# Optimization experiments

Hardware: AMD Instinct MI355X
Metric: run time of the kernel (lower is better)

## Reference

```python
import jax, jax.numpy as jnp
import numpy as np

DECAY = 0.8
BETA = 0.25
EPS = 1e-05
CODEBOOK_SIZE = 16384
CODEBOOK_DIM = 256


def setup_inputs() -> dict:
    key = jax.random.key(0)
    k1, k2 = jax.random.split(key)
    z = jax.random.normal(k1, (16, 256, 32, 32), dtype=jnp.float32)
    # EmbeddingEMA init: weight = randn(K, D) / K; embed_avg = weight.clone(); cluster_size = 0
    weight = jax.random.normal(k2, (CODEBOOK_SIZE, CODEBOOK_DIM), dtype=jnp.float32) / CODEBOOK_SIZE
    cluster_size = jnp.zeros((CODEBOOK_SIZE,), dtype=jnp.float32)
    embed_avg = weight
    return {"z": z, "weight": weight, "cluster_size": cluster_size, "embed_avg": embed_avg}


def reference(z, weight, cluster_size, embed_avg):
    K, D = weight.shape
    # b c h w -> b h w c
    zt = jnp.transpose(z, (0, 2, 3, 1))
    zf = zt.reshape(-1, D)  # [N, D]

    # squared-distance matrix [N, K]: |z|^2 + |w|^2 - 2 z.wT
    d = (jnp.sum(zf * zf, axis=1, keepdims=True)
         + jnp.sum(weight * weight, axis=1)
         - 2.0 * jnp.einsum('nd,kd->nk', zf, weight))
    token = jnp.argmin(d, axis=1)  # [N]

    z_q = weight[token].reshape(zt.shape)  # embedding lookup

    # training-mode EMA updates (scatter-add of one-hot assignments)
    counts = jax.ops.segment_sum(jnp.ones_like(token, dtype=zf.dtype), token, num_segments=K)
    embed_sum = jax.ops.segment_sum(zf, token, num_segments=K)  # one_hot.T @ zf
    cluster_new = DECAY * cluster_size + (1.0 - DECAY) * counts
    embed_avg_new = DECAY * embed_avg + (1.0 - DECAY) * embed_sum
    n = jnp.sum(cluster_new)
    smoothed = (cluster_new + EPS) / (n + K * EPS) * n
    weight_new = embed_avg_new / smoothed[:, None]

    # commitment loss (z_q detached)
    loss = BETA * jnp.mean((jax.lax.stop_gradient(z_q) - zt) ** 2)
    # straight-through estimator
    z_q_ste = zt + jax.lax.stop_gradient(z_q - zt)
    quant_error = jnp.mean(jnp.sum((z_q - zt) ** 2, axis=3))

    # codebook stats
    utilization = jnp.sum((counts > 0).astype(jnp.float32)) / K
    avg_probs = counts / jnp.sum(counts)
    perplexity = jnp.exp(-jnp.sum(avg_probs * jnp.log(avg_probs + 1e-10)))

    out = jnp.transpose(z_q_ste, (0, 3, 1, 2))  # b h w c -> b c h w
    return (out, loss, quant_error, utilization, perplexity,
            weight_new, cluster_new, embed_avg_new)
```

## Files before the change

### kernel.cpp

```cpp
#include <hip/hip_runtime.h>

#define N_TOK 16384
#define KCB   16384
#define DIM   256
#define HW    1024
#define DECAYF 0.8f
#define ONE_M_DECAY 0.2f
#define BETAF 0.25f
#define EPSF  1e-5f
#define STRIPS 8
#define KB_PER 16

typedef __attribute__((ext_vector_type(8))) short bf16x8;
typedef __attribute__((ext_vector_type(4))) float f32x4;

__device__ __forceinline__ float wave_reduce_sum(float s) {
    #pragma unroll
    for (int o = 32; o > 0; o >>= 1) s += __shfl_down(s, o);
    return s;
}

__device__ __forceinline__ unsigned short f2bf(float x) {
    union { float f; unsigned int u; } a; a.f = x;
    unsigned int r = a.u + 0x7fffu + ((a.u >> 16) & 1u);
    return (unsigned short)(r >> 16);
}

__global__ void k_transpose_z(const float* __restrict__ z, float* __restrict__ zf,
                              unsigned short* __restrict__ Ah) {
    __shared__ float t[32][33];
    int b  = blockIdx.z;
    int c0 = blockIdx.y * 32;
    int h0 = blockIdx.x * 32;
    int tid = threadIdx.x;
    int jx = tid & 31, iy = tid >> 5;
    const float* zb = z + (size_t)b * DIM * HW;
    #pragma unroll
    for (int p = 0; p < 4; ++p) {
        int ci = iy + p * 8;
        t[ci][jx] = zb[(size_t)(c0 + ci) * HW + h0 + jx];
    }
    __syncthreads();
    #pragma unroll
    for (int p = 0; p < 4; ++p) {
        int hh = iy + p * 8;
        size_t idx = (size_t)(b * HW + h0 + hh) * DIM + c0 + jx;
        float v = t[jx][hh];
        zf[idx] = v;
        Ah[idx] = f2bf(v);
    }
}

__global__ void k_prep_w(const float* __restrict__ w, unsigned short* __restrict__ Bh,
                         float* __restrict__ wnorm) {
    int wv = blockIdx.x * 4 + (threadIdx.x >> 6);
    int lane = threadIdx.x & 63;
    float4 v = ((const float4*)(w + (size_t)wv * DIM))[lane];
    ushort4 h;
    h.x = f2bf(v.x); h.y = f2bf(v.y); h.z = f2bf(v.z); h.w = f2bf(v.w);
    ((ushort4*)(Bh + (size_t)wv * DIM))[lane] = h;
    float s = v.x * v.x + v.y * v.y + v.z * v.z + v.w * v.w;
    s = wave_reduce_sum(s);
    if (lane == 0) wnorm[wv] = s;
}

__global__ void k_sum_cs(const float* __restrict__ cs, float* __restrict__ scal) {
    int i = blockIdx.x * 256 + threadIdx.x;
    int lane = threadIdx.x & 63;
    float v = cs[i];
    v = wave_reduce_sum(v);
    if (lane == 0) atomicAdd(&scal[1], v);
}

__global__ __launch_bounds__(256) void k_gemm_argmin(
    const unsigned short* __restrict__ Ah, const unsigned short* __restrict__ Bh,
    const float* __restrict__ wnorm, uint2* __restrict__ pout) {
    __shared__ unsigned short As[128 * 256];
    __shared__ unsigned short Bs[128 * 32];

    int tid  = threadIdx.x;
    int wave = tid >> 6, lane = tid & 63;
    int g16  = lane >> 4, r16 = lane & 15;
    int n0   = blockIdx.x * 128;
    int strip = blockIdx.y;

    #pragma unroll
    for (int i = 0; i < 16; ++i) {
        int s = (wave * 16 + i) * 64 + lane;
        int row = s >> 5, pos = s & 31;
        int c = pos ^ (row & 7);
        const unsigned int* ga = (const unsigned int*)(Ah + (size_t)(n0 + row) * 256 + c * 8);
        unsigned int* la = (unsigned int*)&As[(size_t)((wave * 16 + i) * 64) * 8];
        __builtin_amdgcn_global_load_lds((const __attribute__((address_space(1))) unsigned int*)ga,
                                         (__attribute__((address_space(3))) unsigned int*)la, 16, 0, 0);
    }

    unsigned int b1[16], b2[16];
    #pragma unroll
    for (int i = 0; i < 16; ++i) { b1[i] = 0xFFFFFFFFu; b2[i] = 0xFFFFFFFFu; }

    for (int kbi = 0; kbi < KB_PER; ++kbi) {
        int kb = strip * KB_PER + kbi;
        int c0 = kb * 128;

        f32x4 acc[4][4];
        #pragma unroll
        for (int mt = 0; mt < 4; ++mt)
            #pragma unroll
            for (int nt = 0; nt < 4; ++nt)
                acc[mt][nt] = (f32x4){0.f, 0.f, 0.f, 0.f};

        for (int ks = 0; ks < 8; ++ks) {
            __syncthreads();
            #pragma unroll
            for (int j = 0; j < 2; ++j) {
                int s = (wave * 2 + j) * 64 + lane;
                int m = s >> 2, pk = (s & 3) ^ (m & 3);
                const unsigned int* gb = (const unsigned int*)(Bh + (size_t)(c0 + m) * 256 + ks * 32 + pk * 8);
                unsigned int* lb = (unsigned int*)&Bs[(size_t)((wave * 2 + j) * 64) * 8];
                __builtin_amdgcn_global_load_lds((const __attribute__((address_space(1))) unsigned int*)gb,
                                                 (__attribute__((address_space(3))) unsigned int*)lb, 16, 0, 0);
            }
            __syncthreads();
            bf16x8 af[4], bfr[4];
            #pragma unroll
            for (int mt = 0; mt < 4; ++mt) {
                int row = (wave >> 1) * 64 + mt * 16 + r16;
                int pos = (ks * 4 + g16) ^ (row & 7);
                af[mt] = *(const bf16x8*)&As[(row * 32 + pos) * 8];
            }
            #pragma unroll
            for (int nt = 0; nt < 4; ++nt) {
                int row = (wave & 1) * 64 + nt * 16 + r16;
                int pk = g16 ^ (row & 3);
                bfr[nt] = *(const bf16x8*)&Bs[(row * 4 + pk) * 8];
            }
            #pragma unroll
            for (int mt = 0; mt < 4; ++mt)
                #pragma unroll
                for (int nt = 0; nt < 4; ++nt)
                    acc[mt][nt] = __builtin_amdgcn_mfma_f32_16x16x32_bf16(af[mt], bfr[nt], acc[mt][nt], 0, 0, 0);
        }

        float wnb[4];
        unsigned int orv[4];
        #pragma unroll
        for (int nt = 0; nt < 4; ++nt) {
            int code = c0 + (wave & 1) * 64 + nt * 16 + r16;
            wnb[nt] = wnorm[code] + 0.0625f;
            orv[nt] = (unsigned int)((kbi << 7) | ((wave & 1) << 6) | (nt << 4));
        }
        #pragma unroll
        for (int mt = 0; mt < 4; ++mt)
            #pragma unroll
            for (int rg = 0; rg < 4; ++rg) {
                int i = mt * 4 + rg;
                #pragma unroll
                for (int nt = 0; nt < 4; ++nt) {
                    float s = fmaf(-2.0f, acc[mt][nt][rg], wnb[nt]);
                    unsigned int u = (__float_as_uint(s) & 0xFFFFF800u) | orv[nt];
                    unsigned int t = b1[i] > u ? b1[i] : u;
                    b1[i] = b1[i] < u ? b1[i] : u;
                    b2[i] = b2[i] < t ? b2[i] : t;
                }
            }
    }

    #pragma unroll
    for (int i = 0; i < 16; ++i) {
        unsigned int v1 = b1[i] | (unsigned int)r16;
        unsigned int v2 = b2[i] | (unsigned int)r16;
        #pragma unroll
        for (int off = 1; off < 16; off <<= 1) {
            unsigned int o1 = __shfl_xor((int)v1, off);
            unsigned int o2 = __shfl_xor((int)v2, off);
            unsigned int n1 = v1 < o1 ? v1 : o1;
            unsigned int hi = v1 < o1 ? o1 : v1;
            unsigned int lo = v2 < o2 ? v2 : o2;
            v1 = n1;
            v2 = hi < lo ? hi : lo;
        }
        b1[i] = v1; b2[i] = v2;
    }

    __syncthreads();
    unsigned int* red1 = (unsigned int*)Bs;
    unsigned int* red2 = red1 + 256;
    if (r16 == 0) {
        #pragma unroll
        for (int mt = 0; mt < 4; ++mt)
            #pragma unroll
            for (int rg = 0; rg < 4; ++rg) {
                int row = (wave >> 1) * 64 + mt * 16 + g16 * 4 + rg;
                red1[(wave & 1) * 128 + row] = b1[mt * 4 + rg];
                red2[(wave & 1) * 128 + row] = b2[mt * 4 + rg];
            }
    }
    __syncthreads();
    if (tid < 128) {
        unsigned int a1 = red1[tid], a2 = red2[tid];
        unsigned int c1 = red1[128 + tid], c2 = red2[128 + tid];
        unsigned int m1 = a1 < c1 ? a1 : c1;
        unsigned int hi = a1 < c1 ? c1 : a1;
        unsigned int lo = a2 < c2 ? a2 : c2;
        pout[(size_t)strip * N_TOK + n0 + tid] = make_uint2(m1, hi < lo ? hi : lo);
    }
}

__global__ void k_select(const uint2* __restrict__ pout, const float* __restrict__ zf,
                         const float* __restrict__ w, int2* __restrict__ tokrank,
                         float* __restrict__ counts, float* __restrict__ dmin) {
    int n = blockIdx.x * 4 + (threadIdx.x >> 6);
    int lane = threadIdx.x & 63;
    unsigned int c1 = 0xFFFFFFFFu, c2 = 0xFFFFFFFFu;
    int s1 = 0, s2 = 0;
    #pragma unroll
    for (int s = 0; s < STRIPS; ++s) {
        uint2 p = pout[(size_t)s * N_TOK + n];
        if (p.x < c1)      { c2 = c1; s2 = s1; c1 = p.x; s1 = s; }
        else if (p.x < c2) { c2 = p.x; s2 = s; }
        if (p.y < c1)      { c2 = c1; s2 = s1; c1 = p.y; s1 = s; }
        else if (p.y < c2) { c2 = p.y; s2 = s; }
    }
    int code1 = (s1 << 11) | (int)(c1 & 0x7FFu);
    int code2 = (s2 << 11) | (int)(c2 & 0x7FFu);

    float4 zv = ((const float4*)(zf + (size_t)n * DIM))[lane];
    float4 w1 = ((const float4*)(w + (size_t)code1 * DIM))[lane];
    float4 w2 = ((const float4*)(w + (size_t)code2 * DIM))[lane];
    float ax = zv.x - w1.x, ay = zv.y - w1.y, az = zv.z - w1.z, aw = zv.w - w1.w;
    float bx = zv.x - w2.x, by = zv.y - w2.y, bz = zv.z - w2.z, bw = zv.w - w2.w;
    float d1 = ax * ax + ay * ay + az * az + aw * aw;
    float d2 = bx * bx + by * by + bz * bz + bw * bw;
    d1 = wave_reduce_sum(d1);
    d2 = wave_reduce_sum(d2);
    if (lane == 0) {
        bool take2 = (d2 < d1) || (d2 == d1 && code2 < code1);
        int tok = take2 ? code2 : code1;
        dmin[n] = take2 ? d2 : d1;
        float old = atomicAdd(&counts[tok], 1.0f);
        tokrank[n] = make_int2(tok, (int)old);
    }
}

__global__ void k_scan(const float* __restrict__ counts, int* __restrict__ offsets) {
    int tid = threadIdx.x;
    int lane = tid & 63, wv = tid >> 6;
    int base = tid * 64;
    int sum = 0;
    for (int i = 0; i < 64; ++i) sum += (int)counts[base + i];
    int x = sum;
    #pragma unroll
    for (int o = 1; o < 64; o <<= 1) {
        int y = __shfl_up(x, o);
        if (lane >= o) x += y;
    }
    __shared__ int wt[4];
    if (lane == 63) wt[wv] = x;
    __syncthreads();
    int wbase = 0;
    for (int i = 0; i < wv; ++i) wbase += wt[i];
    int run = wbase + x - sum;
    for (int i = 0; i < 64; ++i) {
        offsets[base + i] = run;
        run += (int)counts[base + i];
    }
}

__global__ void k_scatter(const int2* __restrict__ tokrank, const int* __restrict__ offsets,
                          int* __restrict__ perm) {
    int n = blockIdx.x * 256 + threadIdx.x;
    int2 tr = tokrank[n];
    perm[offsets[tr.x] + tr.y] = n;
}

__global__ void k_embed(const int* __restrict__ offsets, const float* __restrict__ counts,
                        const int* __restrict__ perm, const float* __restrict__ zf,
                        const float* __restrict__ ea, const float* __restrict__ cs,
                        const float* __restrict__ scal, float* __restrict__ o_embed,
                        float* __restrict__ o_cluster, float* __restrict__ o_wnew) {
    int k = blockIdx.x * 4 + (threadIdx.x >> 6);
    int lane = threadIdx.x & 63;
    int off = offsets[k];
    int c = (int)counts[k];
    float4 acc = make_float4(0.f, 0.f, 0.f, 0.f);
    for (int i = 0; i < c; ++i) {
        int n = perm[off + i];
        float4 zv = ((const float4*)(zf + (size_t)n * DIM))[lane];
        acc.x += zv.x; acc.y += zv.y; acc.z += zv.z; acc.w += zv.w;
    }
    float4 eav = ((const float4*)(ea + (size_t)k * DIM))[lane];
    float4 em = make_float4(DECAYF * eav.x + ONE_M_DECAY * acc.x,
                            DECAYF * eav.y + ONE_M_DECAY * acc.y,
                            DECAYF * eav.z + ONE_M_DECAY * acc.z,
                            DECAYF * eav.w + ONE_M_DECAY * acc.w);
    ((float4*)(o_embed + (size_t)k * DIM))[lane] = em;
    float cn = DECAYF * cs[k] + ONE_M_DECAY * (float)c;
    float ntot = DECAYF * scal[1] + ONE_M_DECAY * (float)N_TOK;
    float sm = (cn + EPSF) / (ntot + (float)KCB * EPSF) * ntot;
    float inv = 1.0f / sm;
    ((float4*)(o_wnew + (size_t)k * DIM))[lane] =
        make_float4(em.x * inv, em.y * inv, em.z * inv, em.w * inv);
    if (lane == 0) o_cluster[k] = cn;
}

__global__ void k_write_out(const int2* __restrict__ tokrank, const float* __restrict__ w,
                            float* __restrict__ out) {
    __shared__ float t[32][33];
    __shared__ int tok[32];
    int b = blockIdx.z, c0 = blockIdx.y * 32, h0 = blockIdx.x * 32;
    int tid = threadIdx.x, jx = tid & 31, iy = tid >> 5;
    if (tid < 32) tok[tid] = tokrank[b * HW + h0 + tid].x;
    __syncthreads();
    #pragma unroll
    for (int p = 0; p < 4; ++p) {
        int hh = iy + p * 8;
        t[hh][jx] = w[(size_t)tok[hh] * DIM + c0 + jx];
    }
    __syncthreads();
    #pragma unroll
    for (int p = 0; p < 4; ++p) {
        int cc = iy + p * 8;
        out[(size_t)b * DIM * HW + (size_t)(c0 + cc) * HW + h0 + jx] = t[jx][cc];
    }
}

__global__ void k_stats(const float* __restrict__ counts, const float* __restrict__ dmin,
                        float* __restrict__ scal) {
    int k = blockIdx.x * 256 + threadIdx.x;
    int lane = threadIdx.x & 63;
    float cnt = counts[k];
    float used = cnt > 0.f ? 1.f : 0.f;
    float p = cnt * (1.0f / 16384.0f);
    float pl = p * logf(p + 1e-10f);
    float dv = dmin[k];
    used = wave_reduce_sum(used);
    pl   = wave_reduce_sum(pl);
    dv   = wave_reduce_sum(dv);
    if (lane == 0) {
        atomicAdd(&scal[2], used);
        atomicAdd(&scal[3], pl);
        atomicAdd(&scal[0], dv);
    }
}

__global__ void k_scalars(const float* __restrict__ scal, float* __restrict__ o_scal) {
    if (threadIdx.x == 0) {
        float sumsq = scal[0], used = scal[2], plogp = scal[3];
        o_scal[0] = BETAF * sumsq / (float)(N_TOK * DIM);
        o_scal[1] = sumsq / (float)N_TOK;
        o_scal[2] = used * (1.0f / (float)KCB);
        o_scal[3] = expf(-plogp);
    }
}

extern "C" void kernel_launch(void* const* d_in, const int* in_sizes, int n_in,
                              void* d_out, int out_size, void* d_ws, size_t ws_size,
                              hipStream_t stream) {
    const float* z  = (const float*)d_in[0];
    const float* w  = (const float*)d_in[1];
    const float* cs = (const float*)d_in[2];
    const float* ea = (const float*)d_in[3];
    float* out = (float*)d_out;

    char* w8 = (char*)d_ws;
    unsigned short* Ah = (unsigned short*)(w8 + 0);
    unsigned short* Bh = (unsigned short*)(w8 + 8388608);
    float* wnorm   = (float*)(w8 + 16777216);
    int2*  tokrank = (int2*)(w8 + 16842752);
    float* counts  = (float*)(w8 + 16973824);
    int*   offsets = (int*)(w8 + 17039360);
    int*   perm    = (int*)(w8 + 17104896);
    float* scal    = (float*)(w8 + 17170432);
    float* dmin    = (float*)(w8 + 17170496);

    float* zf = out;
    uint2* pout = (uint2*)(out + 4194308);
    float* o_scal    = out + 4194304;
    float* o_wnew    = out + 4194308;
    float* o_cluster = out + 8388612;
    float* o_embed   = out + 8404996;

    hipMemsetAsync(counts, 0, 17170432 + 64 - 16973824, stream);
    k_transpose_z<<<dim3(32, 8, 16), 256, 0, stream>>>(z, zf, Ah);
    k_prep_w<<<4096, 256, 0, stream>>>(w, Bh, wnorm);
    k_sum_cs<<<64, 256, 0, stream>>>(cs, scal);
    k_gemm_argmin<<<dim3(128, STRIPS), 256, 0, stream>>>(Ah, Bh, wnorm, pout);
    k_select<<<4096, 256, 0, stream>>>(pout, zf, w, tokrank, counts, dmin);
    k_scan<<<1, 256, 0, stream>>>(counts, offsets);
    k_scatter<<<64, 256, 0, stream>>>(tokrank, offsets, perm);
    k_embed<<<4096, 256, 0, stream>>>(offsets, counts, perm, zf, ea, cs, scal,
                                      o_embed, o_cluster, o_wnew);
    k_write_out<<<dim3(32, 8, 16), 256, 0, stream>>>(tokrank, w, out);
    k_stats<<<64, 256, 0, stream>>>(counts, dmin, scal);
    k_scalars<<<1, 64, 0, stream>>>(scal, o_scal);
}
```

Measured before the change: 331.8 us.

## Keep A tile in registers and double-buffer codebook tiles in GEMM-argmin

The GEMM-argmin kernel now loads its whole A fragment (token rows) into registers once, instead of staging 64KB in LDS. The codebook B tiles are staged in larger 64-wide K chunks with LDS double buffering, so the next chunk's global loads overlap the current chunk's MFMAs. With LDS use much smaller and launch_bounds(256,2), two blocks can share a CU. The cluster-size sum kernel is folded into the weight prep kernel, saving one launch. The risk is higher register pressure from holding 32 A fragments per thread, which could cause spills.

```diff
diff --git a/kernel.cpp b/kernel.cpp
--- a/kernel.cpp
+++ b/kernel.cpp
@@ -52,31 +52,32 @@
 }
 
 __global__ void k_prep_w(const float* __restrict__ w, unsigned short* __restrict__ Bh,
-                         float* __restrict__ wnorm) {
-    int wv = blockIdx.x * 4 + (threadIdx.x >> 6);
+                         float* __restrict__ wnorm, const float* __restrict__ cs,
+                         float* __restrict__ scal) {
     int lane = threadIdx.x & 63;
-    float4 v = ((const float4*)(w + (size_t)wv * DIM))[lane];
-    ushort4 h;
-    h.x = f2bf(v.x); h.y = f2bf(v.y); h.z = f2bf(v.z); h.w = f2bf(v.w);
-    ((ushort4*)(Bh + (size_t)wv * DIM))[lane] = h;
-    float s = v.x * v.x + v.y * v.y + v.z * v.z + v.w * v.w;
-    s = wave_reduce_sum(s);
-    if (lane == 0) wnorm[wv] = s;
-}
-
-__global__ void k_sum_cs(const float* __restrict__ cs, float* __restrict__ scal) {
-    int i = blockIdx.x * 256 + threadIdx.x;
-    int lane = threadIdx.x & 63;
-    float v = cs[i];
-    v = wave_reduce_sum(v);
-    if (lane == 0) atomicAdd(&scal[1], v);
-}
-
-__global__ __launch_bounds__(256) void k_gemm_argmin(
+    if (blockIdx.x < 4096) {
+        int wv = blockIdx.x * 4 + (threadIdx.x >> 6);
+        float4 v = ((const float4*)(w + (size_t)wv * DIM))[lane];
+        ushort4 h;
+        h.x = f2bf(v.x); h.y = f2bf(v.y); h.z = f2bf(v.z); h.w = f2bf(v.w);
+        ((ushort4*)(Bh + (size_t)wv * DIM))[lane] = h;
+        float s = v.x * v.x + v.y * v.y + v.z * v.z + v.w * v.w;
+        s = wave_reduce_sum(s);
+        if (lane == 0) wnorm[wv] = s;
+    } else {
+        int i = (blockIdx.x - 4096) * 256 + threadIdx.x;
+        float v = cs[i];
+        v = wave_reduce_sum(v);
+        if (lane == 0) atomicAdd(&scal[1], v);
+    }
+}
+
+__global__ __launch_bounds__(256, 2) void k_gemm_argmin(
     const unsigned short* __restrict__ Ah, const unsigned short* __restrict__ Bh,
     const float* __restrict__ wnorm, uint2* __restrict__ pout) {
-    __shared__ unsigned short As[128 * 256];
-    __shared__ unsigned short Bs[128 * 32];
+    __shared__ unsigned short Bs[2][128 * 64];
+    __shared__ unsigned int red1[256];
+    __shared__ unsigned int red2[256];
 
     int tid  = threadIdx.x;
     int wave = tid >> 6, lane = tid & 63;
@@ -84,86 +85,105 @@
     int n0   = blockIdx.x * 128;
     int strip = blockIdx.y;
 
-    #pragma unroll
-    for (int i = 0; i < 16; ++i) {
-        int s = (wave * 16 + i) * 64 + lane;
-        int row = s >> 5, pos = s & 31;
-        int c = pos ^ (row & 7);
-        const unsigned int* ga = (const unsigned int*)(Ah + (size_t)(n0 + row) * 256 + c * 8);
-        unsigned int* la = (unsigned int*)&As[(size_t)((wave * 16 + i) * 64) * 8];
-        __builtin_amdgcn_global_load_lds((const __attribute__((address_space(1))) unsigned int*)ga,
-                                         (__attribute__((address_space(3))) unsigned int*)la, 16, 0, 0);
-    }
+    bf16x8 af[8][4];
+    #pragma unroll
+    for (int ks = 0; ks < 8; ++ks)
+        #pragma unroll
+        for (int mt = 0; mt < 4; ++mt) {
+            int row = n0 + (wave >> 1) * 64 + mt * 16 + r16;
+            af[ks][mt] = *(const bf16x8*)(Ah + (size_t)row * 256 + ks * 32 + g16 * 8);
+        }
 
     unsigned int b1[16], b2[16];
     #pragma unroll
     for (int i = 0; i < 16; ++i) { b1[i] = 0xFFFFFFFFu; b2[i] = 0xFFFFFFFFu; }
 
+    f32x4 acc[4][4];
+    #pragma unroll
+    for (int mt = 0; mt < 4; ++mt)
+        #pragma unroll
+        for (int nt = 0; nt < 4; ++nt)
+            acc[mt][nt] = (f32x4){0.f, 0.f, 0.f, 0.f};
+
+    {
+        int c0 = strip * KB_PER * 128;
+        #pragma unroll
+        for (int i = 0; i < 4; ++i) {
+            int s = i * 256 + tid;
+            int row = s >> 3, sp = (s & 7) ^ (row & 7);
+            const unsigned int* gb = (const unsigned int*)(Bh + (size_t)(c0 + row) * 256 + sp * 8);
+            unsigned int* lb = (unsigned int*)&Bs[0][s * 8];
+            __builtin_amdgcn_global_load_lds((const __attribute__((address_space(1))) unsigned int*)gb,
+                                             (__attribute__((address_space(3))) unsigned int*)lb, 16, 0, 0);
+        }
+    }
+    __syncthreads();
+
     for (int kbi = 0; kbi < KB_PER; ++kbi) {
-        int kb = strip * KB_PER + kbi;
-        int c0 = kb * 128;
-
-        f32x4 acc[4][4];
-        #pragma unroll
-        for (int mt = 0; mt < 4; ++mt)
+        int c0 = (strip * KB_PER + kbi) * 128;
+        #pragma unroll
+        for (int kc = 0; kc < 4; ++kc) {
+            if (kc < 3 || kbi < KB_PER - 1) {
+                int c0n = (kc == 3) ? c0 + 128 : c0;
+                int kcn = (kc + 1) & 3;
+                #pragma unroll
+                for (int i = 0; i < 4; ++i) {
+                    int s = i * 256 + tid;
+                    int row = s >> 3, sp = (s & 7) ^ (row & 7);
+                    const unsigned int* gb =
+                        (const unsigned int*)(Bh + (size_t)(c0n + row) * 256 + kcn * 64 + sp * 8);
+                    unsigned int* lb = (unsigned int*)&Bs[(kc + 1) & 1][s * 8];
+                    __builtin_amdgcn_global_load_lds((const __attribute__((address_space(1))) unsigned int*)gb,
+                                                     (__attribute__((address_space(3))) unsigned int*)lb, 16, 0, 0);
+                }
+            }
             #pragma unroll
-            for (int nt = 0; nt < 4; ++nt)
-                acc[mt][nt] = (f32x4){0.f, 0.f, 0.f, 0.f};
-
-        for (int ks = 0; ks < 8; ++ks) {
-            __syncthreads();
-            #pragma unroll
-            for (int j = 0; j < 2; ++j) {
-                int s = (wave * 2 + j) * 64 + lane;
-                int m = s >> 2, pk = (s & 3) ^ (m & 3);
-                const unsigned int* gb = (const unsigned int*)(Bh + (size_t)(c0 + m) * 256 + ks * 32 + pk * 8);
-                unsigned int* lb = (unsigned int*)&Bs[(size_t)((wave * 2 + j) * 64) * 8];
-                __builtin_amdgcn_global_load_lds((const __attribute__((address_space(1))) unsigned int*)gb,
-                                                 (__attribute__((address_space(3))) unsigned int*)lb, 16, 0, 0);
+            for (int h = 0; h < 2; ++h) {
+                bf16x8 bfr[4];
+                #pragma unroll
+                for (int nt = 0; nt < 4; ++nt) {
+                    int row = (wave & 1) * 64 + nt * 16 + r16;
+                    int sp = (h * 4 + g16) ^ (row & 7);
+                    bfr[nt] = *(const bf16x8*)&Bs[kc & 1][(row * 8 + sp) * 8];
+                }
+                #pragma unroll
+                for (int mt = 0; mt < 4; ++mt)
+                    #pragma unroll
+                    for (int nt = 0; nt < 4; ++nt)
+                        acc[mt][nt] = __builtin_amdgcn_mfma_f32_16x16x32_bf16(
+                            af[kc * 2 + h][mt], bfr[nt], acc[mt][nt], 0, 0, 0);
+            }
+            if (kc == 3) {
+                float wnb[4];
+                unsigned int orv[4];
+                #pragma unroll
+                for (int nt = 0; nt < 4; ++nt) {
+                    int code = c0 + (wave & 1) * 64 + nt * 16 + r16;
+                    wnb[nt] = wnorm[code] + 0.0625f;
+                    orv[nt] = (unsigned int)((kbi << 7) | ((wave & 1) << 6) | (nt << 4));
+                }
+                #pragma unroll
+                for (int mt = 0; mt < 4; ++mt)
+                    #pragma unroll
+                    for (int rg = 0; rg < 4; ++rg) {
+                        int i = mt * 4 + rg;
+                        #pragma unroll
+                        for (int nt = 0; nt < 4; ++nt) {
+                            float s = fmaf(-2.0f, acc[mt][nt][rg], wnb[nt]);
+                            unsigned int u = (__float_as_uint(s) & 0xFFFFF800u) | orv[nt];
+                            unsigned int t = b1[i] > u ? b1[i] : u;
+                            b1[i] = b1[i] < u ? b1[i] : u;
+                            b2[i] = b2[i] < t ? b2[i] : t;
+                        }
+                    }
+                #pragma unroll
+                for (int mt = 0; mt < 4; ++mt)
+                    #pragma unroll
+                    for (int nt = 0; nt < 4; ++nt)
+                        acc[mt][nt] = (f32x4){0.f, 0.f, 0.f, 0.f};
             }
             __syncthreads();
-            bf16x8 af[4], bfr[4];
-            #pragma unroll
-            for (int mt = 0; mt < 4; ++mt) {
-                int row = (wave >> 1) * 64 + mt * 16 + r16;
-                int pos = (ks * 4 + g16) ^ (row & 7);
-                af[mt] = *(const bf16x8*)&As[(row * 32 + pos) * 8];
-            }
-            #pragma unroll
-            for (int nt = 0; nt < 4; ++nt) {
-                int row = (wave & 1) * 64 + nt * 16 + r16;
-                int pk = g16 ^ (row & 3);
-                bfr[nt] = *(const bf16x8*)&Bs[(row * 4 + pk) * 8];
-            }
-            #pragma unroll
-            for (int mt = 0; mt < 4; ++mt)
-                #pragma unroll
-                for (int nt = 0; nt < 4; ++nt)
-                    acc[mt][nt] = __builtin_amdgcn_mfma_f32_16x16x32_bf16(af[mt], bfr[nt], acc[mt][nt], 0, 0, 0);
         }
-
-        float wnb[4];
-        unsigned int orv[4];
-        #pragma unroll
-        for (int nt = 0; nt < 4; ++nt) {
-            int code = c0 + (wave & 1) * 64 + nt * 16 + r16;
-            wnb[nt] = wnorm[code] + 0.0625f;
-            orv[nt] = (unsigned int)((kbi << 7) | ((wave & 1) << 6) | (nt << 4));
-        }
-        #pragma unroll
-        for (int mt = 0; mt < 4; ++mt)
-            #pragma unroll
-            for (int rg = 0; rg < 4; ++rg) {
-                int i = mt * 4 + rg;
-                #pragma unroll
-                for (int nt = 0; nt < 4; ++nt) {
-                    float s = fmaf(-2.0f, acc[mt][nt][rg], wnb[nt]);
-                    unsigned int u = (__float_as_uint(s) & 0xFFFFF800u) | orv[nt];
-                    unsigned int t = b1[i] > u ? b1[i] : u;
-                    b1[i] = b1[i] < u ? b1[i] : u;
-                    b2[i] = b2[i] < t ? b2[i] : t;
-                }
-            }
     }
 
     #pragma unroll
@@ -183,9 +203,6 @@
         b1[i] = v1; b2[i] = v2;
     }
 
-    __syncthreads();
-    unsigned int* red1 = (unsigned int*)Bs;
-    unsigned int* red2 = red1 + 256;
     if (r16 == 0) {
         #pragma unroll
         for (int mt = 0; mt < 4; ++mt)
@@ -383,8 +400,7 @@
 
     hipMemsetAsync(counts, 0, 17170432 + 64 - 16973824, stream);
     k_transpose_z<<<dim3(32, 8, 16), 256, 0, stream>>>(z, zf, Ah);
-    k_prep_w<<<4096, 256, 0, stream>>>(w, Bh, wnorm);
-    k_sum_cs<<<64, 256, 0, stream>>>(cs, scal);
+    k_prep_w<<<4160, 256, 0, stream>>>(w, Bh, wnorm, cs, scal);
     k_gemm_argmin<<<dim3(128, STRIPS), 256, 0, stream>>>(Ah, Bh, wnorm, pout);
     k_select<<<4096, 256, 0, stream>>>(pout, zf, w, tokrank, counts, dmin);
     k_scan<<<1, 256, 0, stream>>>(counts, offsets);
```

After: 415.0 us. 25.1% more time.
